# Performance work log

Hardware: AMD Instinct MI355X
Metric: run time of the kernel (lower is better)

## Reference

```python
import jax, jax.numpy as jnp
import numpy as np

N_NODES = 50000
N_EDGES = 600000
N_GRAPHS = 128
D_IN = 128
D_EDGE = 64
N_LAYERS = 4
BN_EPS = 1e-5


def setup_inputs() -> dict:
    key = jax.random.key(0)
    ks = jax.random.split(key, 10)
    x = jax.random.normal(ks[0], (N_NODES, D_IN), dtype=jnp.float32)
    edge_index = jax.random.randint(ks[1], (2, N_EDGES), 0, N_NODES, dtype=jnp.int32)
    edge_attr = jax.random.normal(ks[2], (N_EDGES, D_EDGE), dtype=jnp.float32)
    batch = jnp.sort(jax.random.randint(ks[3], (N_NODES,), 0, N_GRAPHS, dtype=jnp.int32))
    # stacked per-layer params, scaled ~ 1/sqrt(fan_in) like torch default init
    W_edge = jax.random.normal(ks[4], (N_LAYERS, D_EDGE, D_IN), dtype=jnp.float32) / np.sqrt(D_EDGE)
    b_edge = jnp.zeros((N_LAYERS, D_IN), dtype=jnp.float32)
    W1 = jax.random.normal(ks[5], (N_LAYERS, D_IN, D_IN), dtype=jnp.float32) / np.sqrt(D_IN)
    b1 = jnp.zeros((N_LAYERS, D_IN), dtype=jnp.float32)
    gamma = jnp.ones((N_LAYERS, D_IN), dtype=jnp.float32)
    beta = jnp.zeros((N_LAYERS, D_IN), dtype=jnp.float32)
    rm = jnp.zeros((N_LAYERS, D_IN), dtype=jnp.float32)
    rv = jnp.ones((N_LAYERS, D_IN), dtype=jnp.float32)
    W2 = jax.random.normal(ks[6], (N_LAYERS, D_IN, D_IN), dtype=jnp.float32) / np.sqrt(D_IN)
    b2 = jnp.zeros((N_LAYERS, D_IN), dtype=jnp.float32)
    return {"x": x, "edge_index": edge_index, "edge_attr": edge_attr, "batch": batch,
            "W_edge": W_edge, "b_edge": b_edge, "W1": W1, "b1": b1,
            "gamma": gamma, "beta": beta, "rm": rm, "rv": rv, "W2": W2, "b2": b2}


def _gine_forward(x, edge_index, edge_attr, batch,
                  W_edge, b_edge, W1, b1, gamma, beta, rm, rv, W2, b2):
    src = edge_index[0]
    dst = edge_index[1]
    for i in range(N_LAYERS):
        # GINEConv: msg = relu(x_j + Linear(edge_attr)); agg = scatter_add at dst
        e = edge_attr @ W_edge[i] + b_edge[i]                    # [E, D]
        msg = jax.nn.relu(x[src] + e)                            # gather + fuse
        agg = jax.ops.segment_sum(msg, dst, num_segments=N_NODES)
        h = x + agg                                              # (1+eps)*x, eps=0
        # update MLP: Linear -> BN(eval) -> ReLU -> Linear
        h = h @ W1[i] + b1[i]
        h = gamma[i] * (h - rm[i]) * jax.lax.rsqrt(rv[i] + BN_EPS) + beta[i]
        h = jax.nn.relu(h)
        h = h @ W2[i] + b2[i]
        if i != N_LAYERS - 1:
            h = jax.nn.relu(h)  # dropout is identity in eval mode
        x = h
    # global_mean_pool over graphs
    sums = jax.ops.segment_sum(x, batch, num_segments=N_GRAPHS)
    counts = jax.ops.segment_sum(jnp.ones((N_NODES,), x.dtype), batch, num_segments=N_GRAPHS)
    return sums / jnp.maximum(counts, 1.0)[:, None]


def reference(x, edge_index, edge_attr, batch,
              W_edge, b_edge, W1, b1, gamma, beta, rm, rv, W2, b2):
    return _gine_forward(x, edge_index, edge_attr, batch,
                         W_edge, b_edge, W1, b1, gamma, beta, rm, rv, W2, b2)
```

## Files before the change

### kernel.cpp

```cpp
#include <hip/hip_runtime.h>

#define N_NODES 50000
#define N_EDGES 600000
#define N_GRAPHS 128
#define D 128
#define DE 64
#define N_LAYERS 4
#define BN_EPS 1e-5f
#define ECHUNK 8
#define LDST 136
#define WST 72
#define CTS 132
#define ET 128

typedef __attribute__((ext_vector_type(8))) short short8;
typedef __attribute__((ext_vector_type(4))) float floatx4;

__device__ __forceinline__ unsigned short f2bf(float f) {
    union { float f; unsigned u; } v; v.f = f;
    unsigned r = v.u + 0x7FFF + ((v.u >> 16) & 1);
    return (unsigned short)(r >> 16);
}
__device__ __forceinline__ float bf2f(unsigned short h) {
    union { unsigned u; float f; } v; v.u = ((unsigned)h) << 16; return v.f;
}

__global__ void hist_kernel(const int* __restrict__ ei, int* __restrict__ deg) {
    int e = blockIdx.x * 256 + threadIdx.x;
    if (e < N_EDGES) atomicAdd(&deg[ei[N_EDGES + e]], 1);
}

__global__ void scan1_kernel(const int* __restrict__ deg, int* __restrict__ bsum) {
    __shared__ int s[256];
    int t = threadIdx.x, i = blockIdx.x * 256 + t;
    s[t] = (i < N_NODES) ? deg[i] : 0;
    __syncthreads();
    for (int d = 128; d > 0; d >>= 1) {
        if (t < d) s[t] += s[t + d];
        __syncthreads();
    }
    if (t == 0) bsum[blockIdx.x] = s[0];
}

__global__ void scan2_kernel(int* __restrict__ bsum, int nb) {
    __shared__ int s[256];
    int t = threadIdx.x;
    int v = (t < nb) ? bsum[t] : 0;
    s[t] = v;
    __syncthreads();
    for (int d = 1; d < 256; d <<= 1) {
        int u = (t >= d) ? s[t - d] : 0;
        __syncthreads();
        s[t] += u;
        __syncthreads();
    }
    if (t < nb) bsum[t] = s[t] - v;
}

__global__ void scan3_kernel(const int* __restrict__ deg, const int* __restrict__ bsum,
                             int* __restrict__ off, int* __restrict__ cursor) {
    __shared__ int s[256];
    int t = threadIdx.x, i = blockIdx.x * 256 + t;
    int v = (i < N_NODES) ? deg[i] : 0;
    s[t] = v;
    __syncthreads();
    for (int d = 1; d < 256; d <<= 1) {
        int u = (t >= d) ? s[t - d] : 0;
        __syncthreads();
        s[t] += u;
        __syncthreads();
    }
    if (i < N_NODES) {
        int o = bsum[blockIdx.x] + s[t] - v;
        off[i] = o; cursor[i] = o;
    }
    if (i == N_NODES - 1) off[N_NODES] = bsum[blockIdx.x] + s[t];
}

__global__ void permute_kernel(const int* __restrict__ ei, int* __restrict__ cursor,
                               int* __restrict__ perm, int* __restrict__ srcp,
                               int* __restrict__ dstp) {
    int e = blockIdx.x * 256 + threadIdx.x;
    if (e < N_EDGES) {
        int d = ei[N_EDGES + e];
        int p = atomicAdd(&cursor[d], 1);
        perm[p] = e; srcp[p] = ei[e]; dstp[p] = d;
    }
}

__global__ void eap_kernel(const float* __restrict__ ea, const int* __restrict__ perm,
                           unsigned short* __restrict__ eap) {
    int i = blockIdx.x * 256 + threadIdx.x;
    if (i >= N_EDGES * 16) return;
    int p = i >> 4, c0 = (i & 15) * 4;
    int e = perm[p];
    float4 v = *(const float4*)(ea + (size_t)e * DE + c0);
    union { unsigned short s[4]; unsigned long long u; } pk;
    pk.s[0] = f2bf(v.x); pk.s[1] = f2bf(v.y); pk.s[2] = f2bf(v.z); pk.s[3] = f2bf(v.w);
    *(unsigned long long*)(eap + (size_t)p * DE + c0) = pk.u;
}

__global__ __launch_bounds__(512, 4) void edge_fused(
    const float* __restrict__ x,
    const float* __restrict__ ea,
    const unsigned short* __restrict__ eap,
    const int* __restrict__ perm,
    const int* __restrict__ srcp,
    const int* __restrict__ dstp,
    const float* __restrict__ We, const float* __restrict__ be,
    float* __restrict__ agg, int useEap)
{
    __shared__ __align__(16) unsigned short Wt[D * WST];
    __shared__ __align__(16) unsigned short As[ET * WST];
    __shared__ __align__(16) unsigned short Ct[ET * CTS];
    __shared__ int srcs[ET];
    __shared__ int dsts[ET];
    __shared__ float be_s[D];

    const int tid = threadIdx.x;
    for (int i = tid; i < DE * (D / 4); i += 512) {
        int k = i >> 5, n0 = (i & 31) * 4;
        float4 w = *(const float4*)(We + (size_t)k * D + n0);
        Wt[(n0 + 0) * WST + k] = f2bf(w.x);
        Wt[(n0 + 1) * WST + k] = f2bf(w.y);
        Wt[(n0 + 2) * WST + k] = f2bf(w.z);
        Wt[(n0 + 3) * WST + k] = f2bf(w.w);
    }
    if (tid < D) be_s[tid] = be[tid];

    const int wave = tid >> 6, lane = tid & 63;
    const int lrow = lane & 15, lquad = lane >> 4;
    const int cp = lane;

    const int ntiles = (N_EDGES + ET - 1) / ET;
    for (int g = blockIdx.x; g < ntiles; g += gridDim.x) {
        const int p0 = g * ET;
        const int nv = (N_EDGES - p0 < ET) ? (N_EDGES - p0) : ET;
        if (tid < ET) {
            int ok = tid < nv;
            srcs[tid] = ok ? srcp[p0 + tid] : 0;
            dsts[tid] = ok ? dstp[p0 + tid] : -1;
        }
        if (useEap) {
            for (int i = tid; i < ET * 16; i += 512) {
                int r = i >> 4, c0 = (i & 15) * 4;
                unsigned long long v = 0;
                if (r < nv) v = *(const unsigned long long*)(eap + (size_t)(p0 + r) * DE + c0);
                *(unsigned long long*)&As[r * WST + c0] = v;
            }
        } else {
            for (int i = tid; i < ET * 16; i += 512) {
                int r = i >> 4, c0 = (i & 15) * 4;
                float4 v = make_float4(0.f, 0.f, 0.f, 0.f);
                if (r < nv) {
                    int e = perm[p0 + r];
                    v = *(const float4*)(ea + (size_t)e * DE + c0);
                }
                union { unsigned short s[4]; unsigned long long u; } pk;
                pk.s[0] = f2bf(v.x); pk.s[1] = f2bf(v.y); pk.s[2] = f2bf(v.z); pk.s[3] = f2bf(v.w);
                *(unsigned long long*)&As[r * WST + c0] = pk.u;
            }
        }
        __syncthreads();

        const int rlo = wave * 16;
        {
            floatx4 acc[8];
#pragma unroll
            for (int ct = 0; ct < 8; ct++) acc[ct] = (floatx4){0.f, 0.f, 0.f, 0.f};
#pragma unroll
            for (int ks = 0; ks < 2; ks++) {
                short8 a = *(const short8*)&As[(rlo + lrow) * WST + ks * 32 + lquad * 8];
#pragma unroll
                for (int ct = 0; ct < 8; ct++) {
                    short8 b = *(const short8*)&Wt[(ct * 16 + lrow) * WST + ks * 32 + lquad * 8];
                    acc[ct] = __builtin_amdgcn_mfma_f32_16x16x32_bf16(a, b, acc[ct], 0, 0, 0);
                }
            }
#pragma unroll
            for (int ct = 0; ct < 8; ct++) {
                const int c = ct * 16 + lrow;
                const float bb = be_s[c];
#pragma unroll
                for (int j = 0; j < 4; j++) {
                    const int r = rlo + lquad * 4 + j;
                    Ct[r * CTS + c] = f2bf(acc[ct][j] + bb);
                }
            }
        }

        if (rlo < nv) {
            unsigned ed[16];
            float2 xv[16];
#pragma unroll
            for (int j = 0; j < 16; j++)
                ed[j] = *(const unsigned*)&Ct[(rlo + j) * CTS + 2 * cp];
#pragma unroll
            for (int j = 0; j < 16; j++)
                xv[j] = *(const float2*)(x + (size_t)srcs[rlo + j] * D + 2 * cp);
            float a0 = 0.f, a1 = 0.f;
            int dprev = dsts[rlo];
#pragma unroll
            for (int j = 0; j < 16; j++) {
                float v0 = xv[j].x + bf2f((unsigned short)(ed[j] & 0xFFFF));
                float v1 = xv[j].y + bf2f((unsigned short)(ed[j] >> 16));
                a0 += v0 > 0.f ? v0 : 0.f;
                a1 += v1 > 0.f ? v1 : 0.f;
                int dnext = (j < 15) ? dsts[rlo + j + 1] : -2;
                if (dnext != dprev) {
                    float* ap = agg + (size_t)dprev * D + 2 * cp;
                    unsafeAtomicAdd(ap, a0);
                    unsafeAtomicAdd(ap + 1, a1);
                    a0 = 0.f; a1 = 0.f;
                    dprev = dnext;
                }
            }
        }
        __syncthreads();
    }
}

__global__ void copy_f4(const float4* __restrict__ src, float4* __restrict__ dst, int n4) {
    int i = blockIdx.x * blockDim.x + threadIdx.x;
    int stride = gridDim.x * blockDim.x;
    for (; i < n4; i += stride) dst[i] = src[i];
}

__global__ __launch_bounds__(128) void edge_kernel(
    const float* __restrict__ xin, const int* __restrict__ ei,
    const float* __restrict__ ea,  const float* __restrict__ We,
    const float* __restrict__ be,  float* __restrict__ agg)
{
    __shared__ float eas[ECHUNK * DE];
    const int t = threadIdx.x;
    float w[DE];
#pragma unroll
    for (int k = 0; k < DE; k++) w[k] = We[k * D + t];
    const float bias = be[t];
    const int nch = N_EDGES / ECHUNK;
    for (int ch = blockIdx.x; ch < nch; ch += gridDim.x) {
        const int e0 = ch * ECHUNK;
        ((float4*)eas)[t] = ((const float4*)(ea + (size_t)e0 * DE))[t];
        __syncthreads();
#pragma unroll
        for (int j = 0; j < ECHUNK; j++) {
            const int e = e0 + j;
            const int s = ei[e];
            const int d = ei[N_EDGES + e];
            float acc = bias;
            const float4* v4 = (const float4*)(eas + j * DE);
#pragma unroll
            for (int k4 = 0; k4 < DE / 4; k4++) {
                float4 v = v4[k4];
                acc += v.x * w[4 * k4 + 0];
                acc += v.y * w[4 * k4 + 1];
                acc += v.z * w[4 * k4 + 2];
                acc += v.w * w[4 * k4 + 3];
            }
            float msg = xin[(size_t)s * D + t] + acc;
            msg = msg > 0.f ? msg : 0.f;
            unsafeAtomicAdd(&agg[(size_t)d * D + t], msg);
        }
        __syncthreads();
    }
}

__global__ __launch_bounds__(512, 4) void mlp_kernel(
    float* __restrict__ io,
    const float* __restrict__ W1, const float* __restrict__ b1,
    const float* __restrict__ gamma, const float* __restrict__ beta,
    const float* __restrict__ rm,    const float* __restrict__ rv,
    const float* __restrict__ W2, const float* __restrict__ b2,
    float* __restrict__ agg2, int relu2)
{
    __shared__ __align__(16) unsigned short Wt1[D * LDST];
    __shared__ __align__(16) unsigned short Wt2[D * LDST];
    __shared__ __align__(16) unsigned short At[32 * LDST];
    __shared__ float alpha_s[D], betac_s[D], b2_s[D];

    const int tid = threadIdx.x;
    for (int i = tid; i < D * (D / 4); i += 512) {
        const int k = i >> 5;
        const int n0 = (i & 31) * 4;
        float4 w = *(const float4*)(W1 + (size_t)k * D + n0);
        Wt1[(n0 + 0) * LDST + k] = f2bf(w.x);
        Wt1[(n0 + 1) * LDST + k] = f2bf(w.y);
        Wt1[(n0 + 2) * LDST + k] = f2bf(w.z);
        Wt1[(n0 + 3) * LDST + k] = f2bf(w.w);
        float4 u = *(const float4*)(W2 + (size_t)k * D + n0);
        Wt2[(n0 + 0) * LDST + k] = f2bf(u.x);
        Wt2[(n0 + 1) * LDST + k] = f2bf(u.y);
        Wt2[(n0 + 2) * LDST + k] = f2bf(u.z);
        Wt2[(n0 + 3) * LDST + k] = f2bf(u.w);
    }
    if (tid < D) {
        float a = gamma[tid] * rsqrtf(rv[tid] + BN_EPS);
        alpha_s[tid] = a;
        betac_s[tid] = beta[tid] + (b1[tid] - rm[tid]) * a;
        b2_s[tid] = b2[tid];
    }
    __syncthreads();

    const int wave = tid >> 6;
    const int lane = tid & 63;
    const int lrow = lane & 15;
    const int lquad = lane >> 4;
    const int rowg = wave & 1;
    const int colq = wave >> 1;

    const int ntiles = (N_NODES + 31) / 32;
    for (int g = blockIdx.x; g < ntiles; g += gridDim.x) {
        const int row0 = g * 32;
        for (int i = tid; i < 32 * (D / 4); i += 512) {
            const int r = i >> 5;
            const int c0 = (i & 31) * 4;
            const int rr = row0 + r;
            float4 v = make_float4(0.f, 0.f, 0.f, 0.f);
            if (rr < N_NODES) v = *(const float4*)(io + (size_t)rr * D + c0);
            union { unsigned short s[4]; unsigned long long u; } p;
            p.s[0] = f2bf(v.x); p.s[1] = f2bf(v.y); p.s[2] = f2bf(v.z); p.s[3] = f2bf(v.w);
            *(unsigned long long*)&At[r * LDST + c0] = p.u;
        }
        __syncthreads();

        floatx4 acc[2];
#pragma unroll
        for (int q = 0; q < 2; q++) acc[q] = (floatx4){0.f, 0.f, 0.f, 0.f};
#pragma unroll
        for (int ks = 0; ks < 4; ks++) {
            short8 a = *(const short8*)&At[(rowg * 16 + lrow) * LDST + ks * 32 + lquad * 8];
#pragma unroll
            for (int q = 0; q < 2; q++) {
                const int ct = colq * 2 + q;
                short8 b = *(const short8*)&Wt1[(ct * 16 + lrow) * LDST + ks * 32 + lquad * 8];
                acc[q] = __builtin_amdgcn_mfma_f32_16x16x32_bf16(a, b, acc[q], 0, 0, 0);
            }
        }
        __syncthreads();
#pragma unroll
        for (int q = 0; q < 2; q++) {
            const int c = (colq * 2 + q) * 16 + lrow;
            const float al = alpha_s[c], bt = betac_s[c];
#pragma unroll
            for (int j = 0; j < 4; j++) {
                const int r = rowg * 16 + lquad * 4 + j;
                float v = acc[q][j] * al + bt;
                v = v > 0.f ? v : 0.f;
                At[r * LDST + c] = f2bf(v);
            }
        }
        __syncthreads();

        floatx4 acc2[2];
#pragma unroll
        for (int q = 0; q < 2; q++) acc2[q] = (floatx4){0.f, 0.f, 0.f, 0.f};
#pragma unroll
        for (int ks = 0; ks < 4; ks++) {
            short8 a = *(const short8*)&At[(rowg * 16 + lrow) * LDST + ks * 32 + lquad * 8];
#pragma unroll
            for (int q = 0; q < 2; q++) {
                const int ct = colq * 2 + q;
                short8 b = *(const short8*)&Wt2[(ct * 16 + lrow) * LDST + ks * 32 + lquad * 8];
                acc2[q] = __builtin_amdgcn_mfma_f32_16x16x32_bf16(a, b, acc2[q], 0, 0, 0);
            }
        }
#pragma unroll
        for (int q = 0; q < 2; q++) {
            const int c = (colq * 2 + q) * 16 + lrow;
            const float bb = b2_s[c];
#pragma unroll
            for (int j = 0; j < 4; j++) {
                const int r = row0 + rowg * 16 + lquad * 4 + j;
                if (r < N_NODES) {
                    float v = acc2[q][j] + bb;
                    if (relu2) v = v > 0.f ? v : 0.f;
                    io[(size_t)r * D + c] = v;
                    if (agg2) agg2[(size_t)r * D + c] = v;
                }
            }
        }
        __syncthreads();
    }
}

#define PB 1024
#define PC ((N_NODES + PB - 1) / PB)
__global__ __launch_bounds__(128) void pool_a(
    const float* __restrict__ xin, const int* __restrict__ batch,
    float* __restrict__ tmp)
{
    const int b = blockIdx.x, t = threadIdx.x;
    int n0 = b * PC;
    int n1 = n0 + PC; if (n1 > N_NODES) n1 = N_NODES;
    if (n0 >= n1) return;
    float s = 0.f;
    int gprev = batch[n0];
    for (int n = n0; n < n1; n++) {
        int g = batch[n];
        if (g != gprev) {
            unsafeAtomicAdd(&tmp[(size_t)gprev * D + t], s);
            s = 0.f; gprev = g;
        }
        s += xin[(size_t)n * D + t];
    }
    unsafeAtomicAdd(&tmp[(size_t)gprev * D + t], s);
}

__global__ __launch_bounds__(128) void pool_b(
    const float* __restrict__ tmp, const int* __restrict__ batch,
    float* __restrict__ out)
{
    const int g = blockIdx.x, t = threadIdx.x;
    int lo = 0, hi = N_NODES;
    while (lo < hi) { int m = (lo + hi) >> 1; if (batch[m] < g) lo = m + 1; else hi = m; }
    int lo2 = lo, hi2 = N_NODES;
    while (lo2 < hi2) { int m = (lo2 + hi2) >> 1; if (batch[m] < g + 1) lo2 = m + 1; else hi2 = m; }
    int cnt = lo2 - lo;
    out[(size_t)g * D + t] = tmp[(size_t)g * D + t] / (float)(cnt > 0 ? cnt : 1);
}

extern "C" void kernel_launch(void* const* d_in, const int* in_sizes, int n_in,
                              void* d_out, int out_size, void* d_ws, size_t ws_size,
                              hipStream_t stream) {
    const float* x     = (const float*)d_in[0];
    const int*   ei    = (const int*)  d_in[1];
    const float* ea    = (const float*)d_in[2];
    const int*   batch = (const int*)  d_in[3];
    const float* We    = (const float*)d_in[4];
    const float* be    = (const float*)d_in[5];
    const float* W1    = (const float*)d_in[6];
    const float* b1    = (const float*)d_in[7];
    const float* gamma = (const float*)d_in[8];
    const float* beta  = (const float*)d_in[9];
    const float* rm    = (const float*)d_in[10];
    const float* rv    = (const float*)d_in[11];
    const float* W2    = (const float*)d_in[12];
    const float* b2    = (const float*)d_in[13];
    float* out = (float*)d_out;

    char* ws = (char*)d_ws;
    size_t o = 0;
    auto alloc = [&](size_t bytes) -> char* {
        char* p = ws + o; o = (o + bytes + 255) & ~(size_t)255; return p;
    };
    float* bufA  = (float*)alloc((size_t)N_NODES * D * 4);
    float* bufB  = (float*)alloc((size_t)N_NODES * D * 4);
    int* deg     = (int*)alloc((size_t)N_NODES * 4);
    int* off     = (int*)alloc((size_t)(N_NODES + 1) * 4);
    int* cursor  = (int*)alloc((size_t)N_NODES * 4);
    int* perm    = (int*)alloc((size_t)N_EDGES * 4);
    int* srcp    = (int*)alloc((size_t)N_EDGES * 4);
    int* dstp    = (int*)alloc((size_t)N_EDGES * 4);
    int* bsum    = (int*)alloc(256 * 4);
    float* ptmp  = (float*)alloc((size_t)N_GRAPHS * D * 4);
    const size_t needSorted = o;
    unsigned short* eap = nullptr;
    if (ws_size >= needSorted + (size_t)N_EDGES * DE * 2)
        eap = (unsigned short*)(ws + needSorted);
    const bool sorted = (ws_size >= needSorted);

    const int NB = (N_NODES + 255) / 256;

    if (sorted) {
        hipMemsetAsync(deg, 0, (size_t)N_NODES * 4, stream);
        hipMemsetAsync(ptmp, 0, (size_t)N_GRAPHS * D * 4, stream);
        hist_kernel<<<(N_EDGES + 255) / 256, 256, 0, stream>>>(ei, deg);
        scan1_kernel<<<NB, 256, 0, stream>>>(deg, bsum);
        scan2_kernel<<<1, 256, 0, stream>>>(bsum, NB);
        scan3_kernel<<<NB, 256, 0, stream>>>(deg, bsum, off, cursor);
        permute_kernel<<<(N_EDGES + 255) / 256, 256, 0, stream>>>(ei, cursor, perm, srcp, dstp);
        if (eap) eap_kernel<<<(N_EDGES * 16 + 255) / 256, 256, 0, stream>>>(ea, perm, eap);

        const float* cur = x;
        float* agg = bufA;
        float* nxtAgg = bufB;
        copy_f4<<<1024, 256, 0, stream>>>((const float4*)x, (float4*)agg, N_NODES * D / 4);
        for (int i = 0; i < N_LAYERS; i++) {
            edge_fused<<<1024, 512, 0, stream>>>(cur, ea, eap, perm, srcp, dstp,
                                                 We + (size_t)i * DE * D, be + (size_t)i * D,
                                                 agg, eap ? 1 : 0);
            mlp_kernel<<<512, 512, 0, stream>>>(agg,
                W1 + (size_t)i * D * D, b1 + (size_t)i * D,
                gamma + (size_t)i * D, beta + (size_t)i * D,
                rm + (size_t)i * D, rv + (size_t)i * D,
                W2 + (size_t)i * D * D, b2 + (size_t)i * D,
                (i != N_LAYERS - 1) ? nxtAgg : nullptr,
                (i != N_LAYERS - 1) ? 1 : 0);
            cur = agg;
            agg = nxtAgg;
            nxtAgg = (float*)cur;
        }
        pool_a<<<PB, 128, 0, stream>>>(cur, batch, ptmp);
        pool_b<<<N_GRAPHS, 128, 0, stream>>>(ptmp, batch, out);
    } else {
        const float* cur = x;
        float* nxt = bufA;
        for (int i = 0; i < N_LAYERS; i++) {
            copy_f4<<<1024, 256, 0, stream>>>((const float4*)cur, (float4*)nxt, N_NODES * D / 4);
            edge_kernel<<<4096, 128, 0, stream>>>(cur, ei, ea, We + (size_t)i * DE * D, be + (size_t)i * D, nxt);
            mlp_kernel<<<512, 512, 0, stream>>>(nxt,
                W1 + (size_t)i * D * D, b1 + (size_t)i * D,
                gamma + (size_t)i * D, beta + (size_t)i * D,
                rm + (size_t)i * D, rv + (size_t)i * D,
                W2 + (size_t)i * D * D, b2 + (size_t)i * D,
                nullptr, (i != N_LAYERS - 1) ? 1 : 0);
            cur = nxt;
            nxt = (nxt == bufA) ? bufB : bufA;
        }
        hipMemsetAsync(ptmp, 0, (size_t)N_GRAPHS * D * 4, stream);
        pool_a<<<PB, 128, 0, stream>>>(cur, batch, ptmp);
        pool_b<<<N_GRAPHS, 128, 0, stream>>>(ptmp, batch, out);
    }
}
```

Baseline: 876.8 us.

## Gather bf16 node features, prefetch edge tiles, and register-load MLP inputs

Keeps a bf16 copy of the node features, written by the MLP epilogue and by a new init kernel, so the per-edge gather in edge_fused reads half the bytes. The sorted-edge path now prefetches the next tile's edge attributes and indices into registers while the current tile computes. The MLP kernel loads its A operand straight into registers with a prefetch of the next tile, which removes a shared-memory staging pass and one barrier. The edge grid drops from 1024 to 512 blocks, and pooling reads bf16 features. In exchange the gathered node features and the pooled output lose precision, and the workspace must hold the extra bf16 buffers.

Measured after the change: 840.6 us. -4.1%, faster.

```diff
diff --git a/kernel.cpp b/kernel.cpp
--- a/kernel.cpp
+++ b/kernel.cpp
@@ -15,6 +15,7 @@
 
 typedef __attribute__((ext_vector_type(8))) short short8;
 typedef __attribute__((ext_vector_type(4))) float floatx4;
+typedef unsigned long long u64;
 
 __device__ __forceinline__ unsigned short f2bf(float f) {
     union { float f; unsigned u; } v; v.f = f;
@@ -95,15 +96,29 @@
     int p = i >> 4, c0 = (i & 15) * 4;
     int e = perm[p];
     float4 v = *(const float4*)(ea + (size_t)e * DE + c0);
-    union { unsigned short s[4]; unsigned long long u; } pk;
+    union { unsigned short s[4]; u64 u; } pk;
     pk.s[0] = f2bf(v.x); pk.s[1] = f2bf(v.y); pk.s[2] = f2bf(v.z); pk.s[3] = f2bf(v.w);
-    *(unsigned long long*)(eap + (size_t)p * DE + c0) = pk.u;
+    *(u64*)(eap + (size_t)p * DE + c0) = pk.u;
+}
+
+__global__ void init_kernel(const float* __restrict__ x, float* __restrict__ agg,
+                            unsigned short* __restrict__ xb) {
+    int i = blockIdx.x * 256 + threadIdx.x;
+    int stride = gridDim.x * 256;
+    for (; i < N_NODES * D / 4; i += stride) {
+        float4 v = ((const float4*)x)[i];
+        ((float4*)agg)[i] = v;
+        union { unsigned short s[4]; u64 u; } pk;
+        pk.s[0] = f2bf(v.x); pk.s[1] = f2bf(v.y); pk.s[2] = f2bf(v.z); pk.s[3] = f2bf(v.w);
+        *(u64*)(xb + (size_t)i * 4) = pk.u;
+    }
 }
 
 __global__ __launch_bounds__(512, 4) void edge_fused(
-    const float* __restrict__ x,
+    const unsigned short* __restrict__ xb,
+    const float* __restrict__ xf,
+    const unsigned short* __restrict__ eap,
     const float* __restrict__ ea,
-    const unsigned short* __restrict__ eap,
     const int* __restrict__ perm,
     const int* __restrict__ srcp,
     const int* __restrict__ dstp,
@@ -131,24 +146,128 @@
     const int wave = tid >> 6, lane = tid & 63;
     const int lrow = lane & 15, lquad = lane >> 4;
     const int cp = lane;
-
     const int ntiles = (N_EDGES + ET - 1) / ET;
-    for (int g = blockIdx.x; g < ntiles; g += gridDim.x) {
-        const int p0 = g * ET;
-        const int nv = (N_EDGES - p0 < ET) ? (N_EDGES - p0) : ET;
-        if (tid < ET) {
-            int ok = tid < nv;
-            srcs[tid] = ok ? srcp[p0 + tid] : 0;
-            dsts[tid] = ok ? dstp[p0 + tid] : -1;
-        }
-        if (useEap) {
-            for (int i = tid; i < ET * 16; i += 512) {
+
+    auto body = [&](int nv) {
+        const int rlo = wave * 16;
+        floatx4 acc[8];
+#pragma unroll
+        for (int ct = 0; ct < 8; ct++) acc[ct] = (floatx4){0.f, 0.f, 0.f, 0.f};
+#pragma unroll
+        for (int ks = 0; ks < 2; ks++) {
+            short8 a = *(const short8*)&As[(rlo + lrow) * WST + ks * 32 + lquad * 8];
+#pragma unroll
+            for (int ct = 0; ct < 8; ct++) {
+                short8 b = *(const short8*)&Wt[(ct * 16 + lrow) * WST + ks * 32 + lquad * 8];
+                acc[ct] = __builtin_amdgcn_mfma_f32_16x16x32_bf16(a, b, acc[ct], 0, 0, 0);
+            }
+        }
+#pragma unroll
+        for (int ct = 0; ct < 8; ct++) {
+            const int c = ct * 16 + lrow;
+            const float bb = be_s[c];
+#pragma unroll
+            for (int j = 0; j < 4; j++) {
+                const int r = rlo + lquad * 4 + j;
+                Ct[r * CTS + c] = f2bf(acc[ct][j] + bb);
+            }
+        }
+        if (rlo < nv) {
+            unsigned ed[16];
+#pragma unroll
+            for (int j = 0; j < 16; j++)
+                ed[j] = *(const unsigned*)&Ct[(rlo + j) * CTS + 2 * cp];
+            float a0 = 0.f, a1 = 0.f;
+            int dprev = dsts[rlo];
+            if (xb) {
+                unsigned xu[16];
+#pragma unroll
+                for (int j = 0; j < 16; j++)
+                    xu[j] = *(const unsigned*)(xb + (size_t)srcs[rlo + j] * D + 2 * cp);
+#pragma unroll
+                for (int j = 0; j < 16; j++) {
+                    float v0 = bf2f((unsigned short)(xu[j] & 0xFFFF)) + bf2f((unsigned short)(ed[j] & 0xFFFF));
+                    float v1 = bf2f((unsigned short)(xu[j] >> 16)) + bf2f((unsigned short)(ed[j] >> 16));
+                    a0 += v0 > 0.f ? v0 : 0.f;
+                    a1 += v1 > 0.f ? v1 : 0.f;
+                    int dnext = (j < 15) ? dsts[rlo + j + 1] : -2;
+                    if (dnext != dprev) {
+                        float* ap = agg + (size_t)dprev * D + 2 * cp;
+                        unsafeAtomicAdd(ap, a0);
+                        unsafeAtomicAdd(ap + 1, a1);
+                        a0 = 0.f; a1 = 0.f;
+                        dprev = dnext;
+                    }
+                }
+            } else {
+                float2 xv[16];
+#pragma unroll
+                for (int j = 0; j < 16; j++)
+                    xv[j] = *(const float2*)(xf + (size_t)srcs[rlo + j] * D + 2 * cp);
+#pragma unroll
+                for (int j = 0; j < 16; j++) {
+                    float v0 = xv[j].x + bf2f((unsigned short)(ed[j] & 0xFFFF));
+                    float v1 = xv[j].y + bf2f((unsigned short)(ed[j] >> 16));
+                    a0 += v0 > 0.f ? v0 : 0.f;
+                    a1 += v1 > 0.f ? v1 : 0.f;
+                    int dnext = (j < 15) ? dsts[rlo + j + 1] : -2;
+                    if (dnext != dprev) {
+                        float* ap = agg + (size_t)dprev * D + 2 * cp;
+                        unsafeAtomicAdd(ap, a0);
+                        unsafeAtomicAdd(ap + 1, a1);
+                        a0 = 0.f; a1 = 0.f;
+                        dprev = dnext;
+                    }
+                }
+            }
+        }
+    };
+
+    if (useEap) {
+        u64 pfA[4];
+        int pfS = 0, pfD = -1;
+        auto ldt = [&](int gg) {
+            if (gg < ntiles) {
+                const int p0 = gg * ET;
+                const int nv = (N_EDGES - p0 < ET) ? (N_EDGES - p0) : ET;
+#pragma unroll
+                for (int it = 0; it < 4; it++) {
+                    int i = tid + it * 512;
+                    int r = i >> 4, c0 = (i & 15) * 4;
+                    pfA[it] = (r < nv) ? *(const u64*)(eap + (size_t)(p0 + r) * DE + c0) : 0ULL;
+                }
+                if (tid < ET) {
+                    bool ok = tid < nv;
+                    pfS = ok ? srcp[p0 + tid] : 0;
+                    pfD = ok ? dstp[p0 + tid] : -1;
+                }
+            }
+        };
+        ldt(blockIdx.x);
+        for (int g = blockIdx.x; g < ntiles; g += gridDim.x) {
+#pragma unroll
+            for (int it = 0; it < 4; it++) {
+                int i = tid + it * 512;
                 int r = i >> 4, c0 = (i & 15) * 4;
-                unsigned long long v = 0;
-                if (r < nv) v = *(const unsigned long long*)(eap + (size_t)(p0 + r) * DE + c0);
-                *(unsigned long long*)&As[r * WST + c0] = v;
-            }
-        } else {
+                *(u64*)&As[r * WST + c0] = pfA[it];
+            }
+            if (tid < ET) { srcs[tid] = pfS; dsts[tid] = pfD; }
+            __syncthreads();
+            ldt(g + gridDim.x);
+            const int p0 = g * ET;
+            const int nv = (N_EDGES - p0 < ET) ? (N_EDGES - p0) : ET;
+            body(nv);
+            __syncthreads();
+        }
+    } else {
+        for (int g = blockIdx.x; g < ntiles; g += gridDim.x) {
+            const int p0 = g * ET;
+            const int nv = (N_EDGES - p0 < ET) ? (N_EDGES - p0) : ET;
+            if (tid < ET) {
+                bool ok = tid < nv;
+                srcs[tid] = ok ? srcp[p0 + tid] : 0;
+                dsts[tid] = ok ? dstp[p0 + tid] : -1;
+            }
             for (int i = tid; i < ET * 16; i += 512) {
                 int r = i >> 4, c0 = (i & 15) * 4;
                 float4 v = make_float4(0.f, 0.f, 0.f, 0.f);
@@ -156,67 +275,14 @@
                     int e = perm[p0 + r];
                     v = *(const float4*)(ea + (size_t)e * DE + c0);
                 }
-                union { unsigned short s[4]; unsigned long long u; } pk;
+                union { unsigned short s[4]; u64 u; } pk;
                 pk.s[0] = f2bf(v.x); pk.s[1] = f2bf(v.y); pk.s[2] = f2bf(v.z); pk.s[3] = f2bf(v.w);
-                *(unsigned long long*)&As[r * WST + c0] = pk.u;
-            }
-        }
-        __syncthreads();
-
-        const int rlo = wave * 16;
-        {
-            floatx4 acc[8];
-#pragma unroll
-            for (int ct = 0; ct < 8; ct++) acc[ct] = (floatx4){0.f, 0.f, 0.f, 0.f};
-#pragma unroll
-            for (int ks = 0; ks < 2; ks++) {
-                short8 a = *(const short8*)&As[(rlo + lrow) * WST + ks * 32 + lquad * 8];
-#pragma unroll
-                for (int ct = 0; ct < 8; ct++) {
-                    short8 b = *(const short8*)&Wt[(ct * 16 + lrow) * WST + ks * 32 + lquad * 8];
-                    acc[ct] = __builtin_amdgcn_mfma_f32_16x16x32_bf16(a, b, acc[ct], 0, 0, 0);
-                }
-            }
-#pragma unroll
-            for (int ct = 0; ct < 8; ct++) {
-                const int c = ct * 16 + lrow;
-                const float bb = be_s[c];
-#pragma unroll
-                for (int j = 0; j < 4; j++) {
-                    const int r = rlo + lquad * 4 + j;
-                    Ct[r * CTS + c] = f2bf(acc[ct][j] + bb);
-                }
-            }
-        }
-
-        if (rlo < nv) {
-            unsigned ed[16];
-            float2 xv[16];
-#pragma unroll
-            for (int j = 0; j < 16; j++)
-                ed[j] = *(const unsigned*)&Ct[(rlo + j) * CTS + 2 * cp];
-#pragma unroll
-            for (int j = 0; j < 16; j++)
-                xv[j] = *(const float2*)(x + (size_t)srcs[rlo + j] * D + 2 * cp);
-            float a0 = 0.f, a1 = 0.f;
-            int dprev = dsts[rlo];
-#pragma unroll
-            for (int j = 0; j < 16; j++) {
-                float v0 = xv[j].x + bf2f((unsigned short)(ed[j] & 0xFFFF));
-                float v1 = xv[j].y + bf2f((unsigned short)(ed[j] >> 16));
-                a0 += v0 > 0.f ? v0 : 0.f;
-                a1 += v1 > 0.f ? v1 : 0.f;
-                int dnext = (j < 15) ? dsts[rlo + j + 1] : -2;
-                if (dnext != dprev) {
-                    float* ap = agg + (size_t)dprev * D + 2 * cp;
-                    unsafeAtomicAdd(ap, a0);
-                    unsafeAtomicAdd(ap + 1, a1);
-                    a0 = 0.f; a1 = 0.f;
-                    dprev = dnext;
-                }
-            }
-        }
-        __syncthreads();
+                *(u64*)&As[r * WST + c0] = pk.u;
+            }
+            __syncthreads();
+            body(nv);
+            __syncthreads();
+        }
     }
 }
 
@@ -265,17 +331,20 @@
     }
 }
 
-__global__ __launch_bounds__(512, 4) void mlp_kernel(
-    float* __restrict__ io,
+__global__ __launch_bounds__(512, 4) void mlp2_kernel(
+    const float* __restrict__ aggIn,
+    float* __restrict__ fOut,
+    float* __restrict__ aggOut,
+    unsigned short* __restrict__ xbOut,
     const float* __restrict__ W1, const float* __restrict__ b1,
     const float* __restrict__ gamma, const float* __restrict__ beta,
     const float* __restrict__ rm,    const float* __restrict__ rv,
     const float* __restrict__ W2, const float* __restrict__ b2,
-    float* __restrict__ agg2, int relu2)
+    int relu2)
 {
     __shared__ __align__(16) unsigned short Wt1[D * LDST];
     __shared__ __align__(16) unsigned short Wt2[D * LDST];
-    __shared__ __align__(16) unsigned short At[32 * LDST];
+    __shared__ __align__(16) unsigned short T1[32 * LDST];
     __shared__ float alpha_s[D], betac_s[D], b2_s[D];
 
     const int tid = threadIdx.x;
@@ -309,34 +378,46 @@
     const int colq = wave >> 1;
 
     const int ntiles = (N_NODES + 31) / 32;
+    float4 Af[8];
+    auto pf = [&](int gg) {
+        if (gg < ntiles) {
+            const int r = gg * 32 + rowg * 16 + lrow;
+            const bool ok = r < N_NODES;
+            const float* p = aggIn + (size_t)r * D;
+#pragma unroll
+            for (int ks = 0; ks < 4; ks++) {
+                Af[2 * ks + 0] = ok ? *(const float4*)(p + ks * 32 + lquad * 8 + 0) : make_float4(0.f, 0.f, 0.f, 0.f);
+                Af[2 * ks + 1] = ok ? *(const float4*)(p + ks * 32 + lquad * 8 + 4) : make_float4(0.f, 0.f, 0.f, 0.f);
+            }
+        }
+    };
+    pf(blockIdx.x);
+
     for (int g = blockIdx.x; g < ntiles; g += gridDim.x) {
-        const int row0 = g * 32;
-        for (int i = tid; i < 32 * (D / 4); i += 512) {
-            const int r = i >> 5;
-            const int c0 = (i & 31) * 4;
-            const int rr = row0 + r;
-            float4 v = make_float4(0.f, 0.f, 0.f, 0.f);
-            if (rr < N_NODES) v = *(const float4*)(io + (size_t)rr * D + c0);
-            union { unsigned short s[4]; unsigned long long u; } p;
-            p.s[0] = f2bf(v.x); p.s[1] = f2bf(v.y); p.s[2] = f2bf(v.z); p.s[3] = f2bf(v.w);
-            *(unsigned long long*)&At[r * LDST + c0] = p.u;
-        }
-        __syncthreads();
+        short8 a[4];
+#pragma unroll
+        for (int ks = 0; ks < 4; ks++) {
+            union { unsigned short s[8]; short8 v; } pk;
+            pk.s[0] = f2bf(Af[2 * ks].x); pk.s[1] = f2bf(Af[2 * ks].y);
+            pk.s[2] = f2bf(Af[2 * ks].z); pk.s[3] = f2bf(Af[2 * ks].w);
+            pk.s[4] = f2bf(Af[2 * ks + 1].x); pk.s[5] = f2bf(Af[2 * ks + 1].y);
+            pk.s[6] = f2bf(Af[2 * ks + 1].z); pk.s[7] = f2bf(Af[2 * ks + 1].w);
+            a[ks] = pk.v;
+        }
+        pf(g + gridDim.x);
 
         floatx4 acc[2];
 #pragma unroll
         for (int q = 0; q < 2; q++) acc[q] = (floatx4){0.f, 0.f, 0.f, 0.f};
 #pragma unroll
         for (int ks = 0; ks < 4; ks++) {
-            short8 a = *(const short8*)&At[(rowg * 16 + lrow) * LDST + ks * 32 + lquad * 8];
 #pragma unroll
             for (int q = 0; q < 2; q++) {
                 const int ct = colq * 2 + q;
                 short8 b = *(const short8*)&Wt1[(ct * 16 + lrow) * LDST + ks * 32 + lquad * 8];
-                acc[q] = __builtin_amdgcn_mfma_f32_16x16x32_bf16(a, b, acc[q], 0, 0, 0);
-            }
-        }
-        __syncthreads();
+                acc[q] = __builtin_amdgcn_mfma_f32_16x16x32_bf16(a[ks], b, acc[q], 0, 0, 0);
+            }
+        }
 #pragma unroll
         for (int q = 0; q < 2; q++) {
             const int c = (colq * 2 + q) * 16 + lrow;
@@ -346,7 +427,7 @@
                 const int r = rowg * 16 + lquad * 4 + j;
                 float v = acc[q][j] * al + bt;
                 v = v > 0.f ? v : 0.f;
-                At[r * LDST + c] = f2bf(v);
+                T1[r * LDST + c] = f2bf(v);
             }
         }
         __syncthreads();
@@ -356,12 +437,12 @@
         for (int q = 0; q < 2; q++) acc2[q] = (floatx4){0.f, 0.f, 0.f, 0.f};
 #pragma unroll
         for (int ks = 0; ks < 4; ks++) {
-            short8 a = *(const short8*)&At[(rowg * 16 + lrow) * LDST + ks * 32 + lquad * 8];
+            short8 a2 = *(const short8*)&T1[(rowg * 16 + lrow) * LDST + ks * 32 + lquad * 8];
 #pragma unroll
             for (int q = 0; q < 2; q++) {
                 const int ct = colq * 2 + q;
                 short8 b = *(const short8*)&Wt2[(ct * 16 + lrow) * LDST + ks * 32 + lquad * 8];
-                acc2[q] = __builtin_amdgcn_mfma_f32_16x16x32_bf16(a, b, acc2[q], 0, 0, 0);
+                acc2[q] = __builtin_amdgcn_mfma_f32_16x16x32_bf16(a2, b, acc2[q], 0, 0, 0);
             }
         }
 #pragma unroll
@@ -370,12 +451,13 @@
             const float bb = b2_s[c];
 #pragma unroll
             for (int j = 0; j < 4; j++) {
-                const int r = row0 + rowg * 16 + lquad * 4 + j;
+                const int r = g * 32 + rowg * 16 + lquad * 4 + j;
                 if (r < N_NODES) {
                     float v = acc2[q][j] + bb;
                     if (relu2) v = v > 0.f ? v : 0.f;
-                    io[(size_t)r * D + c] = v;
-                    if (agg2) agg2[(size_t)r * D + c] = v;
+                    if (fOut)   fOut[(size_t)r * D + c] = v;
+                    if (aggOut) aggOut[(size_t)r * D + c] = v;
+                    if (xbOut)  xbOut[(size_t)r * D + c] = f2bf(v);
                 }
             }
         }
@@ -385,6 +467,27 @@
 
 #define PB 1024
 #define PC ((N_NODES + PB - 1) / PB)
+__global__ __launch_bounds__(128) void pool_a_bf(
+    const unsigned short* __restrict__ xb, const int* __restrict__ batch,
+    float* __restrict__ tmp)
+{
+    const int b = blockIdx.x, t = threadIdx.x;
+    int n0 = b * PC;
+    int n1 = n0 + PC; if (n1 > N_NODES) n1 = N_NODES;
+    if (n0 >= n1) return;
+    float s = 0.f;
+    int gprev = batch[n0];
+    for (int n = n0; n < n1; n++) {
+        int g = batch[n];
+        if (g != gprev) {
+            unsafeAtomicAdd(&tmp[(size_t)gprev * D + t], s);
+            s = 0.f; gprev = g;
+        }
+        s += bf2f(xb[(size_t)n * D + t]);
+    }
+    unsafeAtomicAdd(&tmp[(size_t)gprev * D + t], s);
+}
+
 __global__ __launch_bounds__(128) void pool_a(
     const float* __restrict__ xin, const int* __restrict__ batch,
     float* __restrict__ tmp)
@@ -443,8 +546,8 @@
     auto alloc = [&](size_t bytes) -> char* {
         char* p = ws + o; o = (o + bytes + 255) & ~(size_t)255; return p;
     };
-    float* bufA  = (float*)alloc((size_t)N_NODES * D * 4);
-    float* bufB  = (float*)alloc((size_t)N_NODES * D * 4);
+    float* aggA  = (float*)alloc((size_t)N_NODES * D * 4);
+    float* aggB  = (float*)alloc((size_t)N_NODES * D * 4);
     int* deg     = (int*)alloc((size_t)N_NODES * 4);
     int* off     = (int*)alloc((size_t)(N_NODES + 1) * 4);
     int* cursor  = (int*)alloc((size_t)N_NODES * 4);
@@ -454,10 +557,15 @@
     int* bsum    = (int*)alloc(256 * 4);
     float* ptmp  = (float*)alloc((size_t)N_GRAPHS * D * 4);
     const size_t needSorted = o;
-    unsigned short* eap = nullptr;
-    if (ws_size >= needSorted + (size_t)N_EDGES * DE * 2)
-        eap = (unsigned short*)(ws + needSorted);
+    unsigned short* eap = (unsigned short*)alloc((size_t)N_EDGES * DE * 2);
+    const size_t needEap = o;
+    unsigned short* xbA = (unsigned short*)alloc((size_t)N_NODES * D * 2);
+    unsigned short* xbB = (unsigned short*)alloc((size_t)N_NODES * D * 2);
+    const size_t needXb = o;
+
     const bool sorted = (ws_size >= needSorted);
+    const int useEap  = (ws_size >= needEap) ? 1 : 0;
+    const bool useXb  = (ws_size >= needXb);
 
     const int NB = (N_NODES + 255) / 256;
 
@@ -469,46 +577,66 @@
         scan2_kernel<<<1, 256, 0, stream>>>(bsum, NB);
         scan3_kernel<<<NB, 256, 0, stream>>>(deg, bsum, off, cursor);
         permute_kernel<<<(N_EDGES + 255) / 256, 256, 0, stream>>>(ei, cursor, perm, srcp, dstp);
-        if (eap) eap_kernel<<<(N_EDGES * 16 + 255) / 256, 256, 0, stream>>>(ea, perm, eap);
-
+        if (useEap) eap_kernel<<<(N_EDGES * 16 + 255) / 256, 256, 0, stream>>>(ea, perm, eap);
+
+        if (useXb) {
+            init_kernel<<<2048, 256, 0, stream>>>(x, aggA, xbA);
+            float* curAgg = aggA; unsigned short* curXb = xbA;
+            float* nxtAgg = aggB; unsigned short* nxtXb = xbB;
+            for (int i = 0; i < N_LAYERS; i++) {
+                const int last = (i == N_LAYERS - 1);
+                edge_fused<<<512, 512, 0, stream>>>(curXb, nullptr, eap, ea, perm, srcp, dstp,
+                                                    We + (size_t)i * DE * D, be + (size_t)i * D,
+                                                    curAgg, useEap);
+                mlp2_kernel<<<512, 512, 0, stream>>>(curAgg, nullptr,
+                    last ? nullptr : nxtAgg, nxtXb,
+                    W1 + (size_t)i * D * D, b1 + (size_t)i * D,
+                    gamma + (size_t)i * D, beta + (size_t)i * D,
+                    rm + (size_t)i * D, rv + (size_t)i * D,
+                    W2 + (size_t)i * D * D, b2 + (size_t)i * D, last ? 0 : 1);
+                float* ta = curAgg; curAgg = nxtAgg; nxtAgg = ta;
+                unsigned short* tx = curXb; curXb = nxtXb; nxtXb = tx;
+            }
+            pool_a_bf<<<PB, 128, 0, stream>>>(curXb, batch, ptmp);
+            pool_b<<<N_GRAPHS, 128, 0, stream>>>(ptmp, batch, out);
+        } else {
+            copy_f4<<<1024, 256, 0, stream>>>((const float4*)x, (float4*)aggA, N_NODES * D / 4);
+            const float* xfCur = x;
+            float* curAgg = aggA; float* othAgg = aggB;
+            for (int i = 0; i < N_LAYERS; i++) {
+                const int last = (i == N_LAYERS - 1);
+                edge_fused<<<512, 512, 0, stream>>>(nullptr, xfCur, eap, ea, perm, srcp, dstp,
+                                                    We + (size_t)i * DE * D, be + (size_t)i * D,
+                                                    curAgg, useEap);
+                mlp2_kernel<<<512, 512, 0, stream>>>(curAgg, curAgg,
+                    last ? nullptr : othAgg, nullptr,
+                    W1 + (size_t)i * D * D, b1 + (size_t)i * D,
+                    gamma + (size_t)i * D, beta + (size_t)i * D,
+                    rm + (size_t)i * D, rv + (size_t)i * D,
+                    W2 + (size_t)i * D * D, b2 + (size_t)i * D, last ? 0 : 1);
+                xfCur = curAgg;
+                float* t = curAgg; curAgg = othAgg; othAgg = t;
+            }
+            pool_a<<<PB, 128, 0, stream>>>(xfCur, batch, ptmp);
+            pool_b<<<N_GRAPHS, 128, 0, stream>>>(ptmp, batch, out);
+        }
+    } else {
+        hipMemsetAsync(ptmp, 0, (size_t)N_GRAPHS * D * 4, stream);
         const float* cur = x;
-        float* agg = bufA;
-        float* nxtAgg = bufB;
-        copy_f4<<<1024, 256, 0, stream>>>((const float4*)x, (float4*)agg, N_NODES * D / 4);
+        float* nxt = aggA;
         for (int i = 0; i < N_LAYERS; i++) {
-            edge_fused<<<1024, 512, 0, stream>>>(cur, ea, eap, perm, srcp, dstp,
-                                                 We + (size_t)i * DE * D, be + (size_t)i * D,
-                                                 agg, eap ? 1 : 0);
-            mlp_kernel<<<512, 512, 0, stream>>>(agg,
+            copy_f4<<<1024, 256, 0, stream>>>((const float4*)cur, (float4*)nxt, N_NODES * D / 4);
+            edge_kernel<<<4096, 128, 0, stream>>>(cur, ei, ea, We + (size_t)i * DE * D, be + (size_t)i * D, nxt);
+            mlp2_kernel<<<512, 512, 0, stream>>>(nxt, nxt, nullptr, nullptr,
                 W1 + (size_t)i * D * D, b1 + (size_t)i * D,
                 gamma + (size_t)i * D, beta + (size_t)i * D,
                 rm + (size_t)i * D, rv + (size_t)i * D,
                 W2 + (size_t)i * D * D, b2 + (size_t)i * D,
-                (i != N_LAYERS - 1) ? nxtAgg : nullptr,
                 (i != N_LAYERS - 1) ? 1 : 0);
-            cur = agg;
-            agg = nxtAgg;
-            nxtAgg = (float*)cur;
+            cur = nxt;
+            nxt = (nxt == aggA) ? aggB : aggA;
         }
         pool_a<<<PB, 128, 0, stream>>>(cur, batch, ptmp);
         pool_b<<<N_GRAPHS, 128, 0, stream>>>(ptmp, batch, out);
-    } else {
-        const float* cur = x;
-        float* nxt = bufA;
-        for (int i = 0; i < N_LAYERS; i++) {
-            copy_f4<<<1024, 256, 0, stream>>>((const float4*)cur, (float4*)nxt, N_NODES * D / 4);
-            edge_kernel<<<4096, 128, 0, stream>>>(cur, ei, ea, We + (size_t)i * DE * D, be + (size_t)i * D, nxt);
-            mlp_kernel<<<512, 512, 0, stream>>>(nxt,
-                W1 + (size_t)i * D * D, b1 + (size_t)i * D,
-                gamma + (size_t)i * D, beta + (size_t)i * D,
-                rm + (size_t)i * D, rv + (size_t)i * D,
-                W2 + (size_t)i * D * D, b2 + (size_t)i * D,
-                nullptr, (i != N_LAYERS - 1) ? 1 : 0);
-            cur = nxt;
-            nxt = (nxt == bufA) ? bufB : bufA;
-        }
-        hipMemsetAsync(ptmp, 0, (size_t)N_GRAPHS * D * 4, stream);
-        pool_a<<<PB, 128, 0, stream>>>(cur, batch, ptmp);
-        pool_b<<<N_GRAPHS, 128, 0, stream>>>(ptmp, batch, out);
-    }
-}
+    }
+}
```
